# Kernel optimization log

Measured on AMD Instinct MI355X. Metric: run time of the kernel, lower is better.

The kernel has to match this reference:

```python
import jax, jax.numpy as jnp
import numpy as np

B = 65536
META = 128
GIN = 2 * META          # gate_input_dim = meta_dim * 2
EOUT = 64               # expert_out_dim
H1, H2 = 128, 64        # expert_hidden_units
GH = 64                 # gate_hidden_units[0]
T1, T2 = 64, 32         # tower_hidden_units
RANK = 8                # feature_gate_rank
NTASK = 4
NEXP_TOTAL = 6          # 2 shared + 2 per group * 2 groups
NEXP_TASK = 4           # 2 shared + 2 group
TASK_TO_GROUP = [0, 0, 1, 1]
LN_EPS = 1e-5


def swish(x):
    return x * jax.nn.sigmoid(x)


def setup_inputs() -> dict:
    key = jax.random.key(0)
    ks = iter(jax.random.split(key, 40))

    def rn(shape, scale=0.05):
        return (jax.random.normal(next(ks), shape, dtype=jnp.float32) * scale)

    inp = {
        'z_meta_shared': jax.random.normal(next(ks), (B, META), dtype=jnp.float32),
        'z_meta_group_0': jax.random.normal(next(ks), (B, META), dtype=jnp.float32),
        'z_meta_group_1': jax.random.normal(next(ks), (B, META), dtype=jnp.float32),
        'v': jax.random.normal(next(ks), (B, GIN), dtype=jnp.float32),
        # stacked experts: order [shared0, shared1, g0e0, g0e1, g1e0, g1e1]
        'exp_W1': rn((NEXP_TOTAL, GIN, H1)), 'exp_b1': rn((NEXP_TOTAL, H1)),
        'exp_W2': rn((NEXP_TOTAL, H1, H2)), 'exp_b2': rn((NEXP_TOTAL, H2)),
        'exp_W3': rn((NEXP_TOTAL, H2, EOUT)), 'exp_b3': rn((NEXP_TOTAL, EOUT)),
        'exp_ln_s': jnp.ones((NEXP_TOTAL, EOUT), jnp.float32),
        'exp_ln_b': jnp.zeros((NEXP_TOTAL, EOUT), jnp.float32),
        # per-task LoRA feature gates
        'fg_A': rn((NTASK, GIN, RANK)), 'fg_B': rn((NTASK, RANK, GIN)),
        # per-task routing gates (GIN -> GH -> NEXP_TASK)
        'tg_W1': rn((NTASK, GIN, GH)), 'tg_b1': rn((NTASK, GH)),
        'tg_W2': rn((NTASK, GH, NEXP_TASK)), 'tg_b2': rn((NTASK, NEXP_TASK)),
        # per-task self gates (EOUT -> NEXP_TASK)
        'sg_W': rn((NTASK, EOUT, NEXP_TASK)), 'sg_b': rn((NTASK, NEXP_TASK)),
        # per-task towers (EOUT -> T1 -> T2 -> 1, final sigmoid)
        'tw_W1': rn((NTASK, EOUT, T1)), 'tw_b1': rn((NTASK, T1)),
        'tw_W2': rn((NTASK, T1, T2)), 'tw_b2': rn((NTASK, T2)),
        'tw_W3': rn((NTASK, T2, 1)), 'tw_b3': rn((NTASK, 1)),
    }
    return inp


def reference(z_meta_shared, z_meta_group_0, z_meta_group_1, v,
              exp_W1, exp_b1, exp_W2, exp_b2, exp_W3, exp_b3, exp_ln_s, exp_ln_b,
              fg_A, fg_B, tg_W1, tg_b1, tg_W2, tg_b2, sg_W, sg_b,
              tw_W1, tw_b1, tw_W2, tw_b2, tw_W3, tw_b3):
    groups = [z_meta_group_0, z_meta_group_1]
    diag_idx = jnp.arange(NEXP_TASK)
    preds = []
    for t in range(NTASK):  # small fixed task loop (structurally distinct params)
        g = TASK_TO_GROUP[t]
        cm = jnp.concatenate([z_meta_shared, groups[g]], axis=1)  # [B, GIN]
        # feature gate: 2 * sigmoid(LoRA(cm))
        gate = 2.0 * jax.nn.sigmoid((cm @ fg_A[t]) @ fg_B[t])
        cm = cm * gate
        # experts for this task: 2 shared + 2 group experts
        eidx = jnp.array([0, 1, 2 + 2 * g, 3 + 2 * g])
        h = swish(jnp.einsum('bi,eih->beh', cm, exp_W1[eidx]) + exp_b1[eidx])
        h = swish(jnp.einsum('beh,eho->beo', h, exp_W2[eidx]) + exp_b2[eidx])
        e = jnp.einsum('beh,eho->beo', h, exp_W3[eidx]) + exp_b3[eidx]  # [B,4,EOUT]
        mu = jnp.mean(e, axis=-1, keepdims=True)
        var = jnp.mean((e - mu) ** 2, axis=-1, keepdims=True)
        e = (e - mu) * jax.lax.rsqrt(var + LN_EPS) * exp_ln_s[eidx] + exp_ln_b[eidx]
        # self gate: diagonal of [B,4,4] logits (note: no activation applied, per source)
        sg_logits = jnp.einsum('beo,ok->bek', e, sg_W[t]) + sg_b[t]
        sw = sg_logits[:, diag_idx, diag_idx]  # [B,4]
        e = e * sw[:, :, None]
        # task routing gate with softmax over experts
        gh = swish(cm @ tg_W1[t] + tg_b1[t])
        gw = jax.nn.softmax(gh @ tg_W2[t] + tg_b2[t], axis=1)[:, :, None]
        agg = jnp.sum(e * gw, axis=1)  # [B, EOUT]
        # tower
        th = swish(agg @ tw_W1[t] + tw_b1[t])
        th = swish(th @ tw_W2[t] + tw_b2[t])
        preds.append(jax.nn.sigmoid(th @ tw_W3[t] + tw_b3[t]))
    return jnp.concatenate(preds, axis=1)  # [B, NTASK]
```

## Files before the change

### kernel.cpp

```cpp
#include <hip/hip_runtime.h>

typedef unsigned short u16;
typedef unsigned int   u32;
typedef __bf16 bf16x8 __attribute__((ext_vector_type(8)));
typedef float  f32x4  __attribute__((ext_vector_type(4)));

#define OFF_W2  196608
#define OFF_W3  245760
#define OFF_TG  270336
#define OFF_TW1 335872
#define OFF_TW2 352256
#define OFF_FGA 360448
#define OFF_FGB 376832
#define NPACK   409600

__device__ __forceinline__ u16 f2bf(float f) {
  union { __bf16 b; u16 u; } cv;
  cv.b = (__bf16)f;
  return cv.u;
}
__device__ __forceinline__ u32 f2bf2(float lo, float hi) {
  return (u32)f2bf(lo) | ((u32)f2bf(hi) << 16);
}
__device__ __forceinline__ float bf2f(u16 s) { return __uint_as_float(((u32)s) << 16); }
__device__ __forceinline__ float bflo(u32 p) { return __uint_as_float(p << 16); }
__device__ __forceinline__ float bfhi(u32 p) { return __uint_as_float(p & 0xffff0000u); }

union U4 { uint4 u; bf16x8 v; };
__device__ __forceinline__ bf16x8 ld_frag(const u16* p) {
  U4 t; t.u = *(const uint4*)p; return t.v;
}
__device__ __forceinline__ f32x4 mfma16(bf16x8 a, bf16x8 b, f32x4 c) {
  return __builtin_amdgcn_mfma_f32_16x16x32_bf16(a, b, c, 0, 0, 0);
}
__device__ __forceinline__ float swishf(float x) { return x / (1.f + __expf(-x)); }
__device__ __forceinline__ float sig2(float x) { return 2.f / (1.f + __expf(-x)); }

__global__ __launch_bounds__(256) void prep_pack(
    const float* __restrict__ eW1, const float* __restrict__ eW2,
    const float* __restrict__ eW3, const float* __restrict__ tgW1,
    const float* __restrict__ twW1, const float* __restrict__ twW2,
    const float* __restrict__ fgA, const float* __restrict__ fgB,
    u16* __restrict__ pk)
{
  int idx = blockIdx.x * 256 + threadIdx.x;
  if (idx >= NPACK) return;
  float v;
  if (idx < OFF_W2) {
    int i = idx & 7, lane = (idx >> 3) & 63, kt = (idx >> 9) & 7, nt = (idx >> 12) & 7, e = idx >> 15;
    int k = kt*32 + (lane>>4)*8 + i, n = nt*16 + (lane & 15);
    v = eW1[(e*256 + k)*128 + n];
  } else if (idx < OFF_W3) {
    int j = idx - OFF_W2;
    int i = j & 7, lane = (j >> 3) & 63, kt = (j >> 9) & 3, nt = (j >> 11) & 3, e = j >> 13;
    int k = kt*32 + (lane>>4)*8 + i, n = nt*16 + (lane & 15);
    v = eW2[(e*128 + k)*64 + n];
  } else if (idx < OFF_TG) {
    int j = idx - OFF_W3;
    int i = j & 7, lane = (j >> 3) & 63, kt = (j >> 9) & 1, nt = (j >> 10) & 3, e = j >> 12;
    int k = kt*32 + (lane>>4)*8 + i, n = nt*16 + (lane & 15);
    v = eW3[(e*64 + k)*64 + n];
  } else if (idx < OFF_TW1) {
    int j = idx - OFF_TG;
    int i = j & 7, lane = (j >> 3) & 63, kt = (j >> 9) & 7, nt = (j >> 12) & 3, t = j >> 14;
    int k = kt*32 + (lane>>4)*8 + i, n = nt*16 + (lane & 15);
    v = tgW1[(t*256 + k)*64 + n];
  } else if (idx < OFF_TW2) {
    int j = idx - OFF_TW1;
    int i = j & 7, lane = (j >> 3) & 63, kt = (j >> 9) & 1, nt = (j >> 10) & 3, t = j >> 12;
    int k = kt*32 + (lane>>4)*8 + i, n = nt*16 + (lane & 15);
    v = twW1[(t*64 + k)*64 + n];
  } else if (idx < OFF_FGA) {
    int j = idx - OFF_TW2;
    int i = j & 7, lane = (j >> 3) & 63, kt = (j >> 9) & 1, nt = (j >> 10) & 1, t = j >> 11;
    int k = kt*32 + (lane>>4)*8 + i, n = nt*16 + (lane & 15);
    v = twW2[(t*64 + k)*32 + n];
  } else if (idx < OFF_FGB) {
    int j = idx - OFF_FGA;
    int i = j & 7, lane = (j >> 3) & 63, kt = (j >> 9) & 7, t = j >> 12;
    int m = lane & 15, k = kt*32 + (lane>>4)*8 + i;
    v = (m < 8) ? fgA[(t*256 + k)*8 + m] : 0.f;
  } else {
    int j = idx - OFF_FGB;
    int i = j & 7, lane = (j >> 3) & 63, mtl = (j >> 9) & 15, t = j >> 13;
    int m = mtl*16 + (lane & 15), kr = (lane>>4)*8 + i;
    v = (kr < 8) ? fgB[t*2048 + kr*256 + m] : 0.f;
  }
  pk[idx] = f2bf(v);
}

__global__ __launch_bounds__(256, 3) void home_main(
    const float* __restrict__ zs, const float* __restrict__ zg0, const float* __restrict__ zg1,
    const float* __restrict__ tgW2, const float* __restrict__ tgb1, const float* __restrict__ tgb2,
    const float* __restrict__ eb1, const float* __restrict__ eb2, const float* __restrict__ eb3,
    const float* __restrict__ lns, const float* __restrict__ lnb,
    const float* __restrict__ sgW, const float* __restrict__ sgb,
    const float* __restrict__ twb1, const float* __restrict__ twb2,
    const float* __restrict__ twW3, const float* __restrict__ twb3,
    const u16* __restrict__ pk, float* __restrict__ out)
{
  __shared__ __align__(16) u16   cmfrag[4*8*64*8];
  __shared__ __align__(16) u16   h1frag[4*4*64*8];
  __shared__ __align__(16) u16   h2frag[4*2*64*8];
  __shared__ __align__(16) float fbuf[2*32*68];
  __shared__ __align__(16) float gwbuf[256];
  __shared__ __align__(16) float smallw[640];

  float* accT    = (float*)h1frag;
  u16*   aggfrag = h2frag;
  u16*   th1frag = (u16*)fbuf;

  const int tid  = threadIdx.x;
  const int lane = tid & 63;
  const int wid  = tid >> 6;
  const int r    = tid >> 3;
  const int q    = tid & 7;
  const int rowBase = blockIdx.x * 32;
  const int mt_r = r >> 4, r15 = r & 15;
  const int rl   = (lane >> 4) * 4;
  const int l15  = lane & 15;
  const int tkw  = wid >> 1;
  const int chw  = wid & 1;
  const f32x4 fz = {0.f, 0.f, 0.f, 0.f};

  #pragma unroll 1
  for (int pair = 0; pair < 2; ++pair) {
    const int g = pair;
    const int tg0 = g*2 + tkw;

    {
      const float* zsrc = (q < 4)
        ? (zs + (size_t)(rowBase + r) * 128 + q * 32)
        : ((pair ? zg1 : zg0) + (size_t)(rowBase + r) * 128 + (q - 4) * 32);
      #pragma unroll
      for (int h = 0; h < 4; ++h) {
        float4 a = ((const float4*)zsrc)[2*h], b4 = ((const float4*)zsrc)[2*h+1];
        uint4 wv;
        wv.x = f2bf2(a.x, a.y);
        wv.y = f2bf2(a.z, a.w);
        wv.z = f2bf2(b4.x, b4.y);
        wv.w = f2bf2(b4.z, b4.w);
        *(uint4*)&cmfrag[((mt_r*8 + q)*64 + r15 + 16*h)*8] = wv;
        *(uint4*)&cmfrag[(((mt_r+2)*8 + q)*64 + r15 + 16*h)*8] = wv;
      }
    }
    #pragma unroll
    for (int tk = 0; tk < 2; ++tk) {
      int e = tid >> 6, c = tid & 63, half = c >> 5, cl = c & 31;
      smallw[tk*320 + (e*2 + half)*36 + cl] = tgW2[(g*2+tk)*256 + c*4 + e];
    }
    __syncthreads();

    const u16* fgbp = pk + OFF_FGB + (tg0*16 + chw*8)*512 + lane*8;
    U4 afg[4];
    #pragma unroll
    for (int m4 = 0; m4 < 4; ++m4) afg[m4].u = *(const uint4*)(fgbp + m4*512);

    {
      f32x4 d1 = fz;
      const u16* ap = pk + OFF_FGA + (tg0*8)*512 + lane*8;
      #pragma unroll
      for (int kt = 0; kt < 8; ++kt) {
        bf16x8 af = ld_frag(ap + kt*512);
        bf16x8 bf = ld_frag(&cmfrag[(((2*tkw + chw)*8 + kt)*64 + lane)*8]);
        d1 = mfma16(af, bf, d1);
      }
      if (rl < 8) {
        #pragma unroll
        for (int rr = 0; rr < 4; ++rr)
          accT[tkw*272 + (rl + rr)*34 + chw*16 + l15] = d1[rr];
      }
    }
    __syncthreads();

    {
      U4 b0u, b1u;
      if (lane < 16) {
        float v0[8], v1[8];
        #pragma unroll
        for (int i = 0; i < 8; ++i) {
          v0[i] = accT[tkw*272 + i*34 + l15];
          v1[i] = accT[tkw*272 + i*34 + 16 + l15];
        }
        b0u.u.x = f2bf2(v0[0], v0[1]); b0u.u.y = f2bf2(v0[2], v0[3]);
        b0u.u.z = f2bf2(v0[4], v0[5]); b0u.u.w = f2bf2(v0[6], v0[7]);
        b1u.u.x = f2bf2(v1[0], v1[1]); b1u.u.y = f2bf2(v1[2], v1[3]);
        b1u.u.z = f2bf2(v1[4], v1[5]); b1u.u.w = f2bf2(v1[6], v1[7]);
      } else {
        b0u.u = make_uint4(0, 0, 0, 0);
        b1u.u = make_uint4(0, 0, 0, 0);
      }
      const int i0 = rl & 7;
      const int hlo = rl >> 3;
      #pragma unroll
      for (int m8 = 0; m8 < 8; ++m8) {
        int mtile = chw*8 + m8;
        bf16x8 af = (m8 < 4) ? afg[m8].v : ld_frag(fgbp + m8*512);
        f32x4 d0 = mfma16(af, b0u.v, fz);
        f32x4 d1 = mfma16(af, b1u.v, fz);
        int ktc = mtile >> 1;
        int hh  = (mtile & 1)*2 + hlo;
        {
          u16* cp = &cmfrag[(((2*tkw)*8 + ktc)*64 + l15 + 16*hh)*8 + i0];
          u32 za = ((u32*)cp)[0], zb = ((u32*)cp)[1];
          float g0 = sig2(d0[0]), g1 = sig2(d0[1]), g2 = sig2(d0[2]), g3 = sig2(d0[3]);
          ((u32*)cp)[0] = f2bf2(bflo(za)*g0, bfhi(za)*g1);
          ((u32*)cp)[1] = f2bf2(bflo(zb)*g2, bfhi(zb)*g3);
        }
        {
          u16* cp = &cmfrag[(((2*tkw + 1)*8 + ktc)*64 + l15 + 16*hh)*8 + i0];
          u32 za = ((u32*)cp)[0], zb = ((u32*)cp)[1];
          float g0 = sig2(d1[0]), g1 = sig2(d1[1]), g2 = sig2(d1[2]), g3 = sig2(d1[3]);
          ((u32*)cp)[0] = f2bf2(bflo(za)*g0, bfhi(za)*g1);
          ((u32*)cp)[1] = f2bf2(bflo(zb)*g2, bfhi(zb)*g3);
        }
      }
    }
    const u16* wp_tg = pk + OFF_TG + ((tg0*4 + chw*2)*8)*512 + lane*8;
    U4 tgp0, tgp1;
    tgp0.u = *(const uint4*)wp_tg;
    tgp1.u = *(const uint4*)(wp_tg + 4096);
    __syncthreads();

    {
      f32x4 accg[2][2] = { { fz, fz }, { fz, fz } };
      #pragma unroll
      for (int kt = 0; kt < 8; ++kt) {
        bf16x8 b0 = (kt == 0) ? tgp0.v : ld_frag(wp_tg + kt*512);
        bf16x8 b1 = (kt == 0) ? tgp1.v : ld_frag(wp_tg + 4096 + kt*512);
        #pragma unroll
        for (int mtl = 0; mtl < 2; ++mtl) {
          bf16x8 a = ld_frag(&cmfrag[(((2*tkw + mtl)*8 + kt)*64 + lane)*8]);
          accg[mtl][0] = mfma16(a, b0, accg[mtl][0]);
          accg[mtl][1] = mfma16(a, b1, accg[mtl][1]);
        }
      }
      #pragma unroll
      for (int nt2 = 0; nt2 < 2; ++nt2) {
        int colg = (chw*2 + nt2)*16 + l15;
        float bias = tgb1[tg0*64 + colg];
        #pragma unroll
        for (int mtl = 0; mtl < 2; ++mtl)
          #pragma unroll
          for (int rr = 0; rr < 4; ++rr)
            fbuf[(tkw*32 + mtl*16 + rl + rr)*68 + colg] = swishf(accg[mtl][nt2][rr] + bias);
      }
    }
    __syncthreads();

    #pragma unroll
    for (int tk = 0; tk < 2; ++tk) {
      int e = q & 3, half = q >> 2;
      float part = 0.f;
      #pragma unroll
      for (int cj = 0; cj < 8; ++cj) {
        float4 g4 = *(const float4*)&fbuf[(tk*32 + r)*68 + half*32 + cj*4];
        float4 w4 = *(const float4*)&smallw[tk*320 + (e*2 + half)*36 + cj*4];
        part += g4.x*w4.x + g4.y*w4.y + g4.z*w4.z + g4.w*w4.w;
      }
      part += __shfl_xor(part, 4);
      float logit = part + tgb2[(g*2+tk)*4 + e];
      float mx = fmaxf(logit, __shfl_xor(logit, 1));
      mx = fmaxf(mx, __shfl_xor(mx, 2));
      float ex = __expf(logit - mx);
      float sm = ex + __shfl_xor(ex, 1);
      sm += __shfl_xor(sm, 2);
      if (q < 4) gwbuf[tk*128 + r*4 + q] = ex / sm;
    }

    float agg[16];
    #pragma unroll
    for (int c = 0; c < 16; ++c) agg[c] = 0.f;

    const int mL  = tid >> 2;
    const int qc  = tid & 3;
    const int tkL = mL >> 5, mrL = mL & 31;

    #pragma unroll 1
    for (int el = 0; el < 4; ++el) {
      const int ei = (el < 2) ? el : (el + 2*g);

      const u16* w1p = pk + ((ei*8 + 2*wid)*8)*512 + lane*8;
      #pragma unroll 1
      for (int pass = 0; pass < 2; ++pass) {
        f32x4 acc1[2][2] = { { fz, fz }, { fz, fz } };
        #pragma unroll
        for (int kt = 0; kt < 8; ++kt) {
          bf16x8 b0 = ld_frag(w1p + kt*512);
          bf16x8 b1 = ld_frag(w1p + 4096 + kt*512);
          #pragma unroll
          for (int mtl = 0; mtl < 2; ++mtl) {
            bf16x8 a = ld_frag(&cmfrag[(((pass*2 + mtl)*8 + kt)*64 + lane)*8]);
            acc1[mtl][0] = mfma16(a, b0, acc1[mtl][0]);
            acc1[mtl][1] = mfma16(a, b1, acc1[mtl][1]);
          }
        }
        #pragma unroll
        for (int nn = 0; nn < 2; ++nn) {
          int col = (2*wid + nn)*16 + l15;
          float bias = eb1[ei*128 + col];
          int kt2 = col >> 5, h2 = (col >> 3) & 3, i2 = col & 7;
          #pragma unroll
          for (int mtl = 0; mtl < 2; ++mtl)
            #pragma unroll
            for (int rr = 0; rr < 4; ++rr)
              h1frag[(((pass*2 + mtl)*4 + kt2)*64 + rl + rr + 16*h2)*8 + i2] =
                  f2bf(swishf(acc1[mtl][nn][rr] + bias));
        }
      }
      const u16* w2p = pk + OFF_W2 + ((ei*4 + wid)*4)*512 + lane*8;
      U4 w2f0, w2f1;
      w2f0.u = *(const uint4*)w2p;
      w2f1.u = *(const uint4*)(w2p + 512);
      __syncthreads();

      f32x4 acc2[4] = { fz, fz, fz, fz };
      #pragma unroll
      for (int kt = 0; kt < 4; ++kt) {
        bf16x8 b0 = (kt == 0) ? w2f0.v : (kt == 1) ? w2f1.v : ld_frag(w2p + kt*512);
        #pragma unroll
        for (int mt = 0; mt < 4; ++mt) {
          bf16x8 a = ld_frag(&h1frag[((mt*4 + kt)*64 + lane)*8]);
          acc2[mt] = mfma16(a, b0, acc2[mt]);
        }
      }
      const u16* w3p = pk + OFF_W3 + ((ei*4 + wid)*2)*512 + lane*8;
      U4 w3f0, w3f1;
      w3f0.u = *(const uint4*)w3p;
      w3f1.u = *(const uint4*)(w3p + 512);
      {
        int col = wid*16 + l15;
        float bias = eb2[ei*64 + col];
        int kt2 = col >> 5, h2 = (col >> 3) & 3, i2 = col & 7;
        #pragma unroll
        for (int mt = 0; mt < 4; ++mt)
          #pragma unroll
          for (int rr = 0; rr < 4; ++rr)
            h2frag[((mt*2 + kt2)*64 + rl + rr + 16*h2)*8 + i2] = f2bf(swishf(acc2[mt][rr] + bias));
      }
      __syncthreads();

      f32x4 acc3[4] = { fz, fz, fz, fz };
      #pragma unroll
      for (int kt = 0; kt < 2; ++kt) {
        bf16x8 b0 = (kt == 0) ? w3f0.v : w3f1.v;
        #pragma unroll
        for (int mt = 0; mt < 4; ++mt) {
          bf16x8 a = ld_frag(&h2frag[((mt*2 + kt)*64 + lane)*8]);
          acc3[mt] = mfma16(a, b0, acc3[mt]);
        }
      }
      {
        int col = wid*16 + l15;
        float bias = eb3[ei*64 + col];
        #pragma unroll
        for (int mt = 0; mt < 4; ++mt)
          #pragma unroll
          for (int rr = 0; rr < 4; ++rr) {
            int m = mt*16 + rl + rr;
            fbuf[((m >> 5)*32 + (m & 31))*68 + col] = acc3[mt][rr] + bias;
          }
      }
      __syncthreads();

      {
        float v[16];
        #pragma unroll
        for (int cc = 0; cc < 4; ++cc) {
          float4 f = *(const float4*)&fbuf[(tkL*32 + mrL)*68 + qc*16 + cc*4];
          v[cc*4+0] = f.x; v[cc*4+1] = f.y; v[cc*4+2] = f.z; v[cc*4+3] = f.w;
        }
        float s1 = 0.f;
        #pragma unroll
        for (int c = 0; c < 16; ++c) s1 += v[c];
        s1 += __shfl_xor(s1, 1); s1 += __shfl_xor(s1, 2);
        float mu = s1 * (1.f/64.f);
        float s2 = 0.f;
        #pragma unroll
        for (int c = 0; c < 16; ++c) { float d = v[c] - mu; s2 += d*d; }
        s2 += __shfl_xor(s2, 1); s2 += __shfl_xor(s2, 2);
        float rs = rsqrtf(s2 * (1.f/64.f) + 1e-5f);
        const int tgL = g*2 + tkL;
        const float* lsp = lns + ei*64 + qc*16;
        const float* lbp = lnb + ei*64 + qc*16;
        const float* sgp = sgW + (tgL*64 + qc*16)*4 + el;
        float swp = 0.f;
        #pragma unroll
        for (int c = 0; c < 16; ++c) {
          float eh = (v[c] - mu) * rs * lsp[c] + lbp[c];
          v[c] = eh;
          swp += eh * sgp[c*4];
        }
        swp += __shfl_xor(swp, 1); swp += __shfl_xor(swp, 2);
        swp += sgb[tgL*4 + el];
        float fac = swp * gwbuf[tkL*128 + mrL*4 + el];
        #pragma unroll
        for (int c = 0; c < 16; ++c) agg[c] += v[c] * fac;
      }
    }

    {
      #pragma unroll
      for (int jh = 0; jh < 2; ++jh) {
        uint4 wv;
        wv.x = f2bf2(agg[jh*8+0], agg[jh*8+1]);
        wv.y = f2bf2(agg[jh*8+2], agg[jh*8+3]);
        wv.z = f2bf2(agg[jh*8+4], agg[jh*8+5]);
        wv.w = f2bf2(agg[jh*8+6], agg[jh*8+7]);
        int tile = (mL >> 4)*2 + (qc >> 1);
        int slot = (mL & 15) + 16*((qc & 1)*2 + jh);
        *(uint4*)&aggfrag[(tile*64 + slot)*8] = wv;
      }
    }
    const u16* tw1b = pk + OFF_TW1 + ((tg0*4 + chw*2)*2)*512 + lane*8;
    U4 t1f0, t1f1;
    t1f0.u = *(const uint4*)tw1b;
    t1f1.u = *(const uint4*)(tw1b + 1024);
    __syncthreads();

    {
      f32x4 at1[2][2] = { { fz, fz }, { fz, fz } };
      #pragma unroll
      for (int kt = 0; kt < 2; ++kt) {
        bf16x8 b0 = (kt == 0) ? t1f0.v : ld_frag(tw1b + kt*512);
        bf16x8 b1 = (kt == 0) ? t1f1.v : ld_frag(tw1b + 1024 + kt*512);
        #pragma unroll
        for (int mtl = 0; mtl < 2; ++mtl) {
          bf16x8 a = ld_frag(&aggfrag[(((2*tkw + mtl)*2 + kt)*64 + lane)*8]);
          at1[mtl][0] = mfma16(a, b0, at1[mtl][0]);
          at1[mtl][1] = mfma16(a, b1, at1[mtl][1]);
        }
      }
      #pragma unroll
      for (int nt2 = 0; nt2 < 2; ++nt2) {
        int colT = (chw*2 + nt2)*16 + l15;
        float bias = twb1[tg0*64 + colT];
        int ktT = colT >> 5, hT = (colT >> 3) & 3, iT = colT & 7;
        #pragma unroll
        for (int mtl = 0; mtl < 2; ++mtl)
          #pragma unroll
          for (int rr = 0; rr < 4; ++rr)
            th1frag[tkw*2048 + ((mtl*2 + ktT)*64 + rl + rr + 16*hT)*8 + iT] =
                f2bf(swishf(at1[mtl][nt2][rr] + bias));
      }
    }
    __syncthreads();

    if (wid < 2) {
      const int tg = g*2 + wid;
      f32x4 at2[2][2] = { { fz, fz }, { fz, fz } };
      const u16* tw2p = pk + OFF_TW2 + (tg*2*2)*512 + lane*8;
      #pragma unroll
      for (int kt = 0; kt < 2; ++kt) {
        bf16x8 b0 = ld_frag(tw2p + kt*512);
        bf16x8 b1 = ld_frag(tw2p + 1024 + kt*512);
        #pragma unroll
        for (int mtl = 0; mtl < 2; ++mtl) {
          bf16x8 a = ld_frag(&th1frag[wid*2048 + ((mtl*2 + kt)*64 + lane)*8]);
          at2[0][mtl] = mfma16(a, b0, at2[0][mtl]);
          at2[1][mtl] = mfma16(a, b1, at2[1][mtl]);
        }
      }
      float pxs[8];
      #pragma unroll
      for (int nt = 0; nt < 2; ++nt) {
        int colU = nt*16 + l15;
        float b2  = twb2[tg*32 + colU];
        float w3v = twW3[tg*32 + colU];
        #pragma unroll
        for (int mtl = 0; mtl < 2; ++mtl)
          #pragma unroll
          for (int rr = 0; rr < 4; ++rr) {
            float val = swishf(at2[nt][mtl][rr] + b2) * w3v;
            if (nt == 0) pxs[mtl*4 + rr] = val;
            else         pxs[mtl*4 + rr] += val;
          }
      }
      #pragma unroll
      for (int k = 0; k < 8; ++k) {
        pxs[k] += __shfl_xor(pxs[k], 1);
        pxs[k] += __shfl_xor(pxs[k], 2);
        pxs[k] += __shfl_xor(pxs[k], 4);
        pxs[k] += __shfl_xor(pxs[k], 8);
      }
      if (l15 == 0) {
        float b3 = twb3[tg];
        #pragma unroll
        for (int mtl = 0; mtl < 2; ++mtl)
          #pragma unroll
          for (int rr = 0; rr < 4; ++rr) {
            int row = mtl*16 + rl + rr;
            float x = pxs[mtl*4 + rr] + b3;
            out[(size_t)(rowBase + row)*4 + tg] = 1.f / (1.f + __expf(-x));
          }
      }
    }
  }
}

extern "C" void kernel_launch(void* const* d_in, const int* in_sizes, int n_in,
                              void* d_out, int out_size, void* d_ws, size_t ws_size,
                              hipStream_t stream)
{
  (void)in_sizes; (void)n_in; (void)out_size; (void)ws_size;
  const float* zs   = (const float*)d_in[0];
  const float* zg0  = (const float*)d_in[1];
  const float* zg1  = (const float*)d_in[2];
  const float* eW1  = (const float*)d_in[4];
  const float* eb1  = (const float*)d_in[5];
  const float* eW2  = (const float*)d_in[6];
  const float* eb2  = (const float*)d_in[7];
  const float* eW3  = (const float*)d_in[8];
  const float* eb3  = (const float*)d_in[9];
  const float* lns  = (const float*)d_in[10];
  const float* lnb  = (const float*)d_in[11];
  const float* fgA  = (const float*)d_in[12];
  const float* fgB  = (const float*)d_in[13];
  const float* tgW1 = (const float*)d_in[14];
  const float* tgb1 = (const float*)d_in[15];
  const float* tgW2 = (const float*)d_in[16];
  const float* tgb2 = (const float*)d_in[17];
  const float* sgW  = (const float*)d_in[18];
  const float* sgb  = (const float*)d_in[19];
  const float* twW1 = (const float*)d_in[20];
  const float* twb1 = (const float*)d_in[21];
  const float* twW2 = (const float*)d_in[22];
  const float* twb2 = (const float*)d_in[23];
  const float* twW3 = (const float*)d_in[24];
  const float* twb3 = (const float*)d_in[25];

  u16* pkw = (u16*)d_ws;
  float* outp = (float*)d_out;

  prep_pack<<<(NPACK + 255)/256, 256, 0, stream>>>(eW1, eW2, eW3, tgW1, twW1, twW2, fgA, fgB, pkw);
  home_main<<<65536/32, 256, 0, stream>>>(zs, zg0, zg1, tgW2, tgb1, tgb2,
      eb1, eb2, eb3, lns, lnb, sgW, sgb, twb1, twb2, twW3, twb3,
      pkw, outp);
}
```

Measured before the change: 345.9 us.

## Restructure feature-gate and tower stages to cut barriers and LDS round-trips

The feature-gate LoRA product now has each wave compute both row halves and exchange results with cross-lane shuffles instead of a shared-memory transpose plus a barrier. Raw inputs are staged in a scratch buffer and gated into the main fragment buffer, removing the duplicate write. The expert first layer is merged into a single pass over all row tiles, and the next expert's weights are prefetched before the barrier. Tower layer 1 is moved into the two waves that run layer 2, which removes a barrier but leaves half the waves idle for that stage and raises register pressure.

```diff
diff --git a/kernel.cpp b/kernel.cpp
--- a/kernel.cpp
+++ b/kernel.cpp
@@ -22,7 +22,6 @@
 __device__ __forceinline__ u32 f2bf2(float lo, float hi) {
   return (u32)f2bf(lo) | ((u32)f2bf(hi) << 16);
 }
-__device__ __forceinline__ float bf2f(u16 s) { return __uint_as_float(((u32)s) << 16); }
 __device__ __forceinline__ float bflo(u32 p) { return __uint_as_float(p << 16); }
 __device__ __forceinline__ float bfhi(u32 p) { return __uint_as_float(p & 0xffff0000u); }
 
@@ -106,7 +105,7 @@
   __shared__ __align__(16) float gwbuf[256];
   __shared__ __align__(16) float smallw[640];
 
-  float* accT    = (float*)h1frag;
+  u16*   scratch = h1frag;
   u16*   aggfrag = h2frag;
   u16*   th1frag = (u16*)fbuf;
 
@@ -140,8 +139,7 @@
         wv.y = f2bf2(a.z, a.w);
         wv.z = f2bf2(b4.x, b4.y);
         wv.w = f2bf2(b4.z, b4.w);
-        *(uint4*)&cmfrag[((mt_r*8 + q)*64 + r15 + 16*h)*8] = wv;
-        *(uint4*)&cmfrag[(((mt_r+2)*8 + q)*64 + r15 + 16*h)*8] = wv;
+        *(uint4*)&scratch[((mt_r*8 + q)*64 + r15 + 16*h)*8] = wv;
       }
     }
     #pragma unroll
@@ -149,6 +147,10 @@
       int e = tid >> 6, c = tid & 63, half = c >> 5, cl = c & 31;
       smallw[tk*320 + (e*2 + half)*36 + cl] = tgW2[(g*2+tk)*256 + c*4 + e];
     }
+    const u16* ap = pk + OFF_FGA + (tg0*8)*512 + lane*8;
+    U4 fga0, fga1;
+    fga0.u = *(const uint4*)ap;
+    fga1.u = *(const uint4*)(ap + 512);
     __syncthreads();
 
     const u16* fgbp = pk + OFF_FGB + (tg0*16 + chw*8)*512 + lane*8;
@@ -156,41 +158,34 @@
     #pragma unroll
     for (int m4 = 0; m4 < 4; ++m4) afg[m4].u = *(const uint4*)(fgbp + m4*512);
 
+    f32x4 d_lo = fz, d_hi = fz;
+    #pragma unroll
+    for (int kt = 0; kt < 8; ++kt) {
+      bf16x8 af = (kt == 0) ? fga0.v : (kt == 1) ? fga1.v : ld_frag(ap + kt*512);
+      d_lo = mfma16(af, ld_frag(&scratch[((0*8 + kt)*64 + lane)*8]), d_lo);
+      d_hi = mfma16(af, ld_frag(&scratch[((1*8 + kt)*64 + lane)*8]), d_hi);
+    }
+    U4 b0u, b1u;
     {
-      f32x4 d1 = fz;
-      const u16* ap = pk + OFF_FGA + (tg0*8)*512 + lane*8;
-      #pragma unroll
-      for (int kt = 0; kt < 8; ++kt) {
-        bf16x8 af = ld_frag(ap + kt*512);
-        bf16x8 bf = ld_frag(&cmfrag[(((2*tkw + chw)*8 + kt)*64 + lane)*8]);
-        d1 = mfma16(af, bf, d1);
-      }
-      if (rl < 8) {
-        #pragma unroll
-        for (int rr = 0; rr < 4; ++rr)
-          accT[tkw*272 + (rl + rr)*34 + chw*16 + l15] = d1[rr];
-      }
-    }
-    __syncthreads();
-
-    {
-      U4 b0u, b1u;
+      float s0[4], s1[4];
+      #pragma unroll
+      for (int rr = 0; rr < 4; ++rr) {
+        s0[rr] = __shfl(d_lo[rr], l15 + 16, 64);
+        s1[rr] = __shfl(d_hi[rr], l15 + 16, 64);
+      }
       if (lane < 16) {
-        float v0[8], v1[8];
-        #pragma unroll
-        for (int i = 0; i < 8; ++i) {
-          v0[i] = accT[tkw*272 + i*34 + l15];
-          v1[i] = accT[tkw*272 + i*34 + 16 + l15];
-        }
-        b0u.u.x = f2bf2(v0[0], v0[1]); b0u.u.y = f2bf2(v0[2], v0[3]);
-        b0u.u.z = f2bf2(v0[4], v0[5]); b0u.u.w = f2bf2(v0[6], v0[7]);
-        b1u.u.x = f2bf2(v1[0], v1[1]); b1u.u.y = f2bf2(v1[2], v1[3]);
-        b1u.u.z = f2bf2(v1[4], v1[5]); b1u.u.w = f2bf2(v1[6], v1[7]);
+        b0u.u.x = f2bf2(d_lo[0], d_lo[1]); b0u.u.y = f2bf2(d_lo[2], d_lo[3]);
+        b0u.u.z = f2bf2(s0[0], s0[1]);     b0u.u.w = f2bf2(s0[2], s0[3]);
+        b1u.u.x = f2bf2(d_hi[0], d_hi[1]); b1u.u.y = f2bf2(d_hi[2], d_hi[3]);
+        b1u.u.z = f2bf2(s1[0], s1[1]);     b1u.u.w = f2bf2(s1[2], s1[3]);
       } else {
         b0u.u = make_uint4(0, 0, 0, 0);
         b1u.u = make_uint4(0, 0, 0, 0);
       }
-      const int i0 = rl & 7;
+    }
+
+    {
+      const int i0  = rl & 7;
       const int hlo = rl >> 3;
       #pragma unroll
       for (int m8 = 0; m8 < 8; ++m8) {
@@ -201,18 +196,18 @@
         int ktc = mtile >> 1;
         int hh  = (mtile & 1)*2 + hlo;
         {
+          const u16* pp = &scratch[((0*8 + ktc)*64 + l15 + 16*hh)*8 + i0];
+          u32 za = ((const u32*)pp)[0], zb = ((const u32*)pp)[1];
           u16* cp = &cmfrag[(((2*tkw)*8 + ktc)*64 + l15 + 16*hh)*8 + i0];
-          u32 za = ((u32*)cp)[0], zb = ((u32*)cp)[1];
-          float g0 = sig2(d0[0]), g1 = sig2(d0[1]), g2 = sig2(d0[2]), g3 = sig2(d0[3]);
-          ((u32*)cp)[0] = f2bf2(bflo(za)*g0, bfhi(za)*g1);
-          ((u32*)cp)[1] = f2bf2(bflo(zb)*g2, bfhi(zb)*g3);
+          ((u32*)cp)[0] = f2bf2(bflo(za)*sig2(d0[0]), bfhi(za)*sig2(d0[1]));
+          ((u32*)cp)[1] = f2bf2(bflo(zb)*sig2(d0[2]), bfhi(zb)*sig2(d0[3]));
         }
         {
+          const u16* pp = &scratch[((1*8 + ktc)*64 + l15 + 16*hh)*8 + i0];
+          u32 za = ((const u32*)pp)[0], zb = ((const u32*)pp)[1];
           u16* cp = &cmfrag[(((2*tkw + 1)*8 + ktc)*64 + l15 + 16*hh)*8 + i0];
-          u32 za = ((u32*)cp)[0], zb = ((u32*)cp)[1];
-          float g0 = sig2(d1[0]), g1 = sig2(d1[1]), g2 = sig2(d1[2]), g3 = sig2(d1[3]);
-          ((u32*)cp)[0] = f2bf2(bflo(za)*g0, bfhi(za)*g1);
-          ((u32*)cp)[1] = f2bf2(bflo(zb)*g2, bfhi(zb)*g3);
+          ((u32*)cp)[0] = f2bf2(bflo(za)*sig2(d1[0]), bfhi(za)*sig2(d1[1]));
+          ((u32*)cp)[1] = f2bf2(bflo(zb)*sig2(d1[2]), bfhi(zb)*sig2(d1[3]));
         }
       }
     }
@@ -245,6 +240,12 @@
           for (int rr = 0; rr < 4; ++rr)
             fbuf[(tkw*32 + mtl*16 + rl + rr)*68 + colg] = swishf(accg[mtl][nt2][rr] + bias);
       }
+    }
+    U4 w1a, w1b;
+    {
+      const u16* w1p0 = pk + ((0*8 + 2*wid)*8)*512 + lane*8;
+      w1a.u = *(const uint4*)w1p0;
+      w1b.u = *(const uint4*)(w1p0 + 4096);
     }
     __syncthreads();
 
@@ -281,37 +282,35 @@
       const int ei = (el < 2) ? el : (el + 2*g);
 
       const u16* w1p = pk + ((ei*8 + 2*wid)*8)*512 + lane*8;
-      #pragma unroll 1
-      for (int pass = 0; pass < 2; ++pass) {
-        f32x4 acc1[2][2] = { { fz, fz }, { fz, fz } };
-        #pragma unroll
-        for (int kt = 0; kt < 8; ++kt) {
-          bf16x8 b0 = ld_frag(w1p + kt*512);
-          bf16x8 b1 = ld_frag(w1p + 4096 + kt*512);
-          #pragma unroll
-          for (int mtl = 0; mtl < 2; ++mtl) {
-            bf16x8 a = ld_frag(&cmfrag[(((pass*2 + mtl)*8 + kt)*64 + lane)*8]);
-            acc1[mtl][0] = mfma16(a, b0, acc1[mtl][0]);
-            acc1[mtl][1] = mfma16(a, b1, acc1[mtl][1]);
-          }
-        }
-        #pragma unroll
-        for (int nn = 0; nn < 2; ++nn) {
-          int col = (2*wid + nn)*16 + l15;
-          float bias = eb1[ei*128 + col];
-          int kt2 = col >> 5, h2 = (col >> 3) & 3, i2 = col & 7;
-          #pragma unroll
-          for (int mtl = 0; mtl < 2; ++mtl)
-            #pragma unroll
-            for (int rr = 0; rr < 4; ++rr)
-              h1frag[(((pass*2 + mtl)*4 + kt2)*64 + rl + rr + 16*h2)*8 + i2] =
-                  f2bf(swishf(acc1[mtl][nn][rr] + bias));
+      f32x4 acc1[4][2];
+      #pragma unroll
+      for (int mt = 0; mt < 4; ++mt) { acc1[mt][0] = fz; acc1[mt][1] = fz; }
+      #pragma unroll
+      for (int kt = 0; kt < 8; ++kt) {
+        bf16x8 b0 = (kt == 0) ? w1a.v : ld_frag(w1p + kt*512);
+        bf16x8 b1 = (kt == 0) ? w1b.v : ld_frag(w1p + 4096 + kt*512);
+        #pragma unroll
+        for (int mt = 0; mt < 4; ++mt) {
+          bf16x8 a = ld_frag(&cmfrag[((mt*8 + kt)*64 + kt*0 + lane)*8]);
+          acc1[mt][0] = mfma16(a, b0, acc1[mt][0]);
+          acc1[mt][1] = mfma16(a, b1, acc1[mt][1]);
         }
       }
       const u16* w2p = pk + OFF_W2 + ((ei*4 + wid)*4)*512 + lane*8;
       U4 w2f0, w2f1;
       w2f0.u = *(const uint4*)w2p;
       w2f1.u = *(const uint4*)(w2p + 512);
+      #pragma unroll
+      for (int nn = 0; nn < 2; ++nn) {
+        int col = (2*wid + nn)*16 + l15;
+        float bias = eb1[ei*128 + col];
+        int kt2 = col >> 5, h2 = (col >> 3) & 3, i2 = col & 7;
+        #pragma unroll
+        for (int mt = 0; mt < 4; ++mt)
+          #pragma unroll
+          for (int rr = 0; rr < 4; ++rr)
+            h1frag[((mt*4 + kt2)*64 + rl + rr + 16*h2)*8 + i2] = f2bf(swishf(acc1[mt][nn][rr] + bias));
+      }
       __syncthreads();
 
       f32x4 acc2[4] = { fz, fz, fz, fz };
@@ -358,8 +357,14 @@
           #pragma unroll
           for (int rr = 0; rr < 4; ++rr) {
             int m = mt*16 + rl + rr;
-            fbuf[((m >> 5)*32 + (m & 31))*68 + col] = acc3[mt][rr] + bias;
+            fbuf[m*68 + col] = acc3[mt][rr] + bias;
           }
+      }
+      if (el < 3) {
+        int ein = (el + 1 < 2) ? (el + 1) : (el + 1 + 2*g);
+        const u16* w1n = pk + ((ein*8 + 2*wid)*8)*512 + lane*8;
+        w1a.u = *(const uint4*)w1n;
+        w1b.u = *(const uint4*)(w1n + 4096);
       }
       __syncthreads();
 
@@ -367,7 +372,7 @@
         float v[16];
         #pragma unroll
         for (int cc = 0; cc < 4; ++cc) {
-          float4 f = *(const float4*)&fbuf[(tkL*32 + mrL)*68 + qc*16 + cc*4];
+          float4 f = *(const float4*)&fbuf[mL*68 + qc*16 + cc*4];
           v[cc*4+0] = f.x; v[cc*4+1] = f.y; v[cc*4+2] = f.z; v[cc*4+3] = f.w;
         }
         float s1 = 0.f;
@@ -412,42 +417,46 @@
         *(uint4*)&aggfrag[(tile*64 + slot)*8] = wv;
       }
     }
-    const u16* tw1b = pk + OFF_TW1 + ((tg0*4 + chw*2)*2)*512 + lane*8;
-    U4 t1f0, t1f1;
-    t1f0.u = *(const uint4*)tw1b;
-    t1f1.u = *(const uint4*)(tw1b + 1024);
-    __syncthreads();
-
-    {
-      f32x4 at1[2][2] = { { fz, fz }, { fz, fz } };
-      #pragma unroll
-      for (int kt = 0; kt < 2; ++kt) {
-        bf16x8 b0 = (kt == 0) ? t1f0.v : ld_frag(tw1b + kt*512);
-        bf16x8 b1 = (kt == 0) ? t1f1.v : ld_frag(tw1b + 1024 + kt*512);
-        #pragma unroll
-        for (int mtl = 0; mtl < 2; ++mtl) {
-          bf16x8 a = ld_frag(&aggfrag[(((2*tkw + mtl)*2 + kt)*64 + lane)*8]);
-          at1[mtl][0] = mfma16(a, b0, at1[mtl][0]);
-          at1[mtl][1] = mfma16(a, b1, at1[mtl][1]);
-        }
-      }
-      #pragma unroll
-      for (int nt2 = 0; nt2 < 2; ++nt2) {
-        int colT = (chw*2 + nt2)*16 + l15;
-        float bias = twb1[tg0*64 + colT];
-        int ktT = colT >> 5, hT = (colT >> 3) & 3, iT = colT & 7;
-        #pragma unroll
-        for (int mtl = 0; mtl < 2; ++mtl)
-          #pragma unroll
-          for (int rr = 0; rr < 4; ++rr)
-            th1frag[tkw*2048 + ((mtl*2 + ktT)*64 + rl + rr + 16*hT)*8 + iT] =
-                f2bf(swishf(at1[mtl][nt2][rr] + bias));
-      }
+    U4 t1p0, t1p1;
+    const u16* tw1b = pk + OFF_TW1 + ((g*2 + wid)*4*2)*512 + lane*8;
+    if (wid < 2) {
+      t1p0.u = *(const uint4*)tw1b;
+      t1p1.u = *(const uint4*)(tw1b + 1024);
     }
     __syncthreads();
 
     if (wid < 2) {
       const int tg = g*2 + wid;
+      f32x4 at1[2][4];
+      #pragma unroll
+      for (int mtl = 0; mtl < 2; ++mtl)
+        #pragma unroll
+        for (int nt = 0; nt < 4; ++nt) at1[mtl][nt] = fz;
+      #pragma unroll
+      for (int kt = 0; kt < 2; ++kt) {
+        #pragma unroll
+        for (int nt = 0; nt < 4; ++nt) {
+          bf16x8 b0 = (kt == 0 && nt == 0) ? t1p0.v :
+                      (kt == 0 && nt == 1) ? t1p1.v : ld_frag(tw1b + (nt*2 + kt)*512);
+          #pragma unroll
+          for (int mtl = 0; mtl < 2; ++mtl) {
+            bf16x8 a = ld_frag(&aggfrag[(((2*wid + mtl)*2 + kt)*64 + lane)*8]);
+            at1[mtl][nt] = mfma16(a, b0, at1[mtl][nt]);
+          }
+        }
+      }
+      #pragma unroll
+      for (int nt = 0; nt < 4; ++nt) {
+        int colT = nt*16 + l15;
+        float bias = twb1[tg*64 + colT];
+        int ktT = colT >> 5, hT = (colT >> 3) & 3, iT = colT & 7;
+        #pragma unroll
+        for (int mtl = 0; mtl < 2; ++mtl)
+          #pragma unroll
+          for (int rr = 0; rr < 4; ++rr)
+            th1frag[wid*2048 + ((mtl*2 + ktT)*64 + rl + rr + 16*hT)*8 + iT] =
+                f2bf(swishf(at1[mtl][nt][rr] + bias));
+      }
       f32x4 at2[2][2] = { { fz, fz }, { fz, fz } };
       const u16* tw2p = pk + OFF_TW2 + (tg*2*2)*512 + lane*8;
       #pragma unroll
```

New measurement: 589.3 us. 1.7x slower.
